# Kernel optimization log

Measured on AMD Instinct MI355X. Metric: run time of the kernel, lower is better.

The kernel has to match this reference:

```python
import jax, jax.numpy as jnp
import numpy as np
from functools import partial

TAU = 2.0          # leak
VTH = 1.0          # threshold_value
DECAY = 1.0 - 1.0 / TAU  # decay_input=False, v_reset=0: v = v*(1-1/tau) + x
PAD = 3
STRIDE = 1


def heaviside(x):
    # forward of spikingjelly surrogate.ATan (surrogate only changes backward)
    return (x >= 0).astype(x.dtype)


def lif(v, inp):
    """One LIF step: charge, fire, hard reset (v_reset=0)."""
    v = v * DECAY + inp
    s = heaviside(v - VTH)
    v = v * (1.0 - s)
    return v, s


def setup_inputs() -> dict:
    key = jax.random.key(0)
    k1, k2, k3, k4 = jax.random.split(key, 4)
    B, L = 64, 2048
    C, H, NC, K = 128, 256, 10, 7
    x = jax.random.normal(k1, (B, L), dtype=jnp.float32)
    conv_w = jax.random.normal(k2, (C, 1, K), dtype=jnp.float32) * (1.0 / np.sqrt(K))
    W1 = jax.random.normal(k3, (H, C), dtype=jnp.float32) * (1.0 / np.sqrt(C))
    W2 = jax.random.normal(k4, (NC, H), dtype=jnp.float32) * (1.0 / np.sqrt(H))
    return {"x": x, "conv_w": conv_w, "W1": W1, "W2": W2}


def _forward(x, conv_w, W1, W2):
    B = x.shape[0]
    C, H, NC = conv_w.shape[0], W1.shape[0], W2.shape[0]
    # Conv1d(1 -> C): [B, 1, L] -> [B, C, T]
    xc = jax.lax.conv_general_dilated(
        x[:, None, :], conv_w, window_strides=(STRIDE,),
        padding=[(PAD, PAD)], dimension_numbers=("NCH", "OIH", "NCH"))
    T = xc.shape[2]
    xt = jnp.transpose(xc, (2, 0, 1))  # [T, B, C]

    def step(carry, x_t):
        v1, v2, v3, acc = carry
        v1, s1 = lif(v1, x_t)                       # conv LIF  [B, C]
        v2, s2 = lif(v2, s1 @ W1.T)                 # hidden LIF [B, H]
        v3, s3 = lif(v3, s2 @ W2.T)                 # output LIF [B, NC]
        return (v1, v2, v3, acc + s3), None

    zeros = lambda d: jnp.zeros((B, d), dtype=x.dtype)
    init = (zeros(C), zeros(H), zeros(NC), zeros(NC))
    (_, _, _, acc), _ = jax.lax.scan(step, init, xt)
    return acc / T


def reference(x, conv_w, W1, W2):
    return _forward(x, conv_w, W1, W2)
```

## Files before the change

### kernel.cpp

```cpp
#include <hip/hip_runtime.h>
#include <stdint.h>

#define T_STEPS 2048
#define BB 64
#define CC 128
#define HH 256
#define NCLS 10

#define S1_OFF  0
#define DP_OFF  16777216
#define DP2_OFF 16908288
#define S2W_OFF 16924672

typedef int v4i __attribute__((ext_vector_type(4)));

__global__ __launch_bounds__(128) void k01_prep(
    const float* __restrict__ x, const float* __restrict__ cw,
    const float* __restrict__ W1, const float* __restrict__ W2,
    unsigned char* __restrict__ s1, signed char* __restrict__ dp,
    signed char* __restrict__ dp2, float* __restrict__ out) {
  const int bx = blockIdx.x;
  const int tidx = threadIdx.x;

  if (bx < 1024) {
    const int c = tidx;
    const int b = bx & 63;
    const int t0 = (bx >> 6) * 128;
    const int ts = t0 - 64;

    float w[7];
#pragma unroll
    for (int k = 0; k < 7; ++k) w[k] = cw[c * 7 + k];

    const float* xb = x + b * 2048;
    float xw[7];
#pragma unroll
    for (int k = 0; k < 7; ++k) {
      int l = ts + k - 3;
      xw[k] = (l >= 0 && l < 2048) ? xb[l] : 0.0f;
    }

    float v = 0.0f;
#pragma unroll 7
    for (int t = ts; t < t0 + 128; ++t) {
      float u = fmaf(w[0], xw[0],
                fmaf(w[1], xw[1],
                fmaf(w[2], xw[2],
                fmaf(w[3], xw[3],
                fmaf(w[4], xw[4],
                fmaf(w[5], xw[5], w[6] * xw[6]))))));
      v = fmaf(v, 0.5f, u);
      bool sp = (v >= 1.0f);
      if (t >= t0) s1[((size_t)t * BB + b) * CC + c] = (unsigned char)(sp ? 1 : 0);
      if (sp) v = 0.0f;
#pragma unroll
      for (int k = 0; k < 6; ++k) xw[k] = xw[k + 1];
      int ln = t + 4;
      xw[6] = (ln >= 0 && ln < 2048) ? xb[ln] : 0.0f;
    }
  } else if (bx < 1280) {
    const int h = bx - 1024;
    const int c = tidx;
    float w = W1[h * CC + c];
    int q = __float2int_rn(w * 2147483648.0f);
#pragma unroll
    for (int d = 0; d < 3; ++d) {
      int dig = (int)(signed char)(q & 0xff);
      dp[d * (HH * CC) + h * CC + c] = (signed char)dig;
      q = (q - dig) >> 8;
    }
    dp[3 * (HH * CC) + h * CC + c] = (signed char)q;
  } else if (bx < 1296) {
    const int nc = bx - 1280;
#pragma unroll
    for (int half = 0; half < 2; ++half) {
      int cc = half * 128 + tidx;
      float w = (nc < NCLS) ? W2[nc * HH + cc] : 0.0f;
      int q = __float2int_rn(w * 2147483648.0f);
#pragma unroll
      for (int d = 0; d < 3; ++d) {
        int dig = (int)(signed char)(q & 0xff);
        dp2[d * (16 * HH) + nc * HH + cc] = (signed char)dig;
        q = (q - dig) >> 8;
      }
      dp2[3 * (16 * HH) + nc * HH + cc] = (signed char)q;
    }
  } else {
#pragma unroll
    for (int i = 0; i < 5; ++i) out[tidx + 128 * i] = 0.0f;
  }
}

__global__ __launch_bounds__(256, 4) void k2_mfma_lif2(
    const unsigned char* __restrict__ s1, const signed char* __restrict__ dp,
    unsigned int* __restrict__ s2w) {
  const int tid  = threadIdx.x;
  const int lane = tid & 63;
  const int wv   = tid >> 6;
  const int hg   = blockIdx.x;
  const int b    = blockIdx.y;
  const int chunk= blockIdx.z;
  const int t0   = chunk * 256;
  const int nwarm= (chunk == 0) ? 0 : 4;
  const int ts   = t0 - nwarm * 16;
  const int l15  = lane & 15;
  const int lg   = lane >> 4;
  const int nn   = lg >> 1;
  const int hb   = hg * 128 + wv * 32;

  v4i Bf[2][4][2];
#pragma unroll
  for (int n = 0; n < 2; ++n)
#pragma unroll
    for (int d = 0; d < 4; ++d)
#pragma unroll
      for (int kc = 0; kc < 2; ++kc)
        Bf[n][d][kc] = *(const v4i*)(dp + d * (HH * CC) +
                                     (hb + n * 16 + l15) * CC + kc * 64 + lg * 16);

  const unsigned char* ap =
      s1 + ((size_t)(ts + l15) * BB + b) * CC + lg * 16;
  v4i Af0 = *(const v4i*)(ap);
  v4i Af1 = *(const v4i*)(ap + 64);
  ap += 16 * BB * CC;

  const int a4 = l15 * 4;
  float v = 0.0f;

  const int nsub = nwarm + 16;
  for (int s = 0; s < nsub; ++s) {
    const int tb = ts + s * 16;

    v4i Pf0 = *(const v4i*)(ap);
    v4i Pf1 = *(const v4i*)(ap + 64);
    ap += 16 * BB * CC;

    float u0[4], u1[4];
#pragma unroll
    for (int n = 0; n < 2; ++n) {
      v4i a0 = {0, 0, 0, 0}, a1 = {0, 0, 0, 0}, a2 = {0, 0, 0, 0}, a3 = {0, 0, 0, 0};
      a0 = __builtin_amdgcn_mfma_i32_16x16x64_i8(Af0, Bf[n][0][0], a0, 0, 0, 0);
      a1 = __builtin_amdgcn_mfma_i32_16x16x64_i8(Af0, Bf[n][1][0], a1, 0, 0, 0);
      a2 = __builtin_amdgcn_mfma_i32_16x16x64_i8(Af0, Bf[n][2][0], a2, 0, 0, 0);
      a3 = __builtin_amdgcn_mfma_i32_16x16x64_i8(Af0, Bf[n][3][0], a3, 0, 0, 0);
      a0 = __builtin_amdgcn_mfma_i32_16x16x64_i8(Af1, Bf[n][0][1], a0, 0, 0, 0);
      a1 = __builtin_amdgcn_mfma_i32_16x16x64_i8(Af1, Bf[n][1][1], a1, 0, 0, 0);
      a2 = __builtin_amdgcn_mfma_i32_16x16x64_i8(Af1, Bf[n][2][1], a2, 0, 0, 0);
      a3 = __builtin_amdgcn_mfma_i32_16x16x64_i8(Af1, Bf[n][3][1], a3, 0, 0, 0);
#pragma unroll
      for (int r = 0; r < 4; ++r) {
        int hi = a3[r] * 256 + a2[r];
        int lo = a1[r] * 256 + a0[r];
        float u = fmaf((float)hi, 0x1p-15f, (float)lo * 0x1p-31f);
        if (n == 0) u0[r] = u; else u1[r] = u;
      }
    }

    float ua[16];
#pragma unroll
    for (int q = 0; q < 4; ++q) {
      const int addr = a4 + q * 64;
#pragma unroll
      for (int r = 0; r < 4; ++r) {
        int g0 = __builtin_amdgcn_ds_bpermute(addr, __float_as_int(u0[r]));
        int g1 = __builtin_amdgcn_ds_bpermute(addr, __float_as_int(u1[r]));
        ua[q * 4 + r] = __int_as_float(nn ? g1 : g0);
      }
    }

    unsigned sel = 0;
#pragma unroll
    for (int j = 0; j < 16; ++j) {
      v = fmaf(v, 0.5f, ua[j]);
      bool sp = (v >= 1.0f);
      if (sp) v = 0.0f;
      unsigned long long Bm = __ballot(sp);
      if (l15 == j)
        sel = (unsigned)(Bm & 0xFFFFull) |
              ((unsigned)((Bm >> 32) & 0xFFFFull) << 16);
    }

    if (s >= nwarm && lg == 0)
      s2w[((size_t)(tb + l15) * BB + b) * 8 + hg * 4 + wv] = sel;

    Af0 = Pf0; Af1 = Pf1;
  }
}

__global__ __launch_bounds__(64, 4) void k34_gemm3_lif3(
    const unsigned int* __restrict__ s2w, const signed char* __restrict__ dp2,
    float* __restrict__ out) {
  const int lane = threadIdx.x;
  const int l15  = lane & 15;
  const int lg   = lane >> 4;
  const int b    = blockIdx.x;
  const int chunk= blockIdx.y;
  const int t0   = chunk * 32;
  const int nwarm= (chunk == 0) ? 0 : 4;
  const int ts   = t0 - nwarm * 16;

  v4i Bf[4][4];
#pragma unroll
  for (int d = 0; d < 4; ++d)
#pragma unroll
    for (int kc = 0; kc < 4; ++kc)
      Bf[d][kc] = *(const v4i*)(dp2 + d * (16 * HH) + l15 * HH + kc * 64 + lg * 16);

  const uint4* rp = (const uint4*)s2w + ((size_t)(ts + l15) * BB + b) * 2;
  uint4 r0 = rp[0], r1 = rp[1];
  rp += 16 * BB * 2;

  const int a4 = l15 * 4;
  const int hw = (lg & 1) * 16;
  float v = 0.0f, cnt = 0.0f;

  const int nsub = nwarm + 2;
  for (int s = 0; s < nsub; ++s) {
    uint4 p0 = rp[0], p1 = rp[1];
    rp += 16 * BB * 2;

    unsigned rowd[8] = {r0.x, r0.y, r0.z, r0.w, r1.x, r1.y, r1.z, r1.w};

    v4i a0 = {0, 0, 0, 0}, a1 = {0, 0, 0, 0}, a2 = {0, 0, 0, 0}, a3 = {0, 0, 0, 0};
#pragma unroll
    for (int kc = 0; kc < 4; ++kc) {
      unsigned h16 = (rowd[kc * 2 + (lg >> 1)] >> hw) & 0xFFFFu;
      v4i Af;
      Af[0] = (int)(((h16 & 0xFu) * 0x00204081u) & 0x01010101u);
      Af[1] = (int)((((h16 >> 4) & 0xFu) * 0x00204081u) & 0x01010101u);
      Af[2] = (int)((((h16 >> 8) & 0xFu) * 0x00204081u) & 0x01010101u);
      Af[3] = (int)((((h16 >> 12) & 0xFu) * 0x00204081u) & 0x01010101u);
      a0 = __builtin_amdgcn_mfma_i32_16x16x64_i8(Af, Bf[0][kc], a0, 0, 0, 0);
      a1 = __builtin_amdgcn_mfma_i32_16x16x64_i8(Af, Bf[1][kc], a1, 0, 0, 0);
      a2 = __builtin_amdgcn_mfma_i32_16x16x64_i8(Af, Bf[2][kc], a2, 0, 0, 0);
      a3 = __builtin_amdgcn_mfma_i32_16x16x64_i8(Af, Bf[3][kc], a3, 0, 0, 0);
    }

    float u[4];
#pragma unroll
    for (int r = 0; r < 4; ++r) {
      int hi = a3[r] * 256 + a2[r];
      int lo = a1[r] * 256 + a0[r];
      u[r] = fmaf((float)hi, 0x1p-15f, (float)lo * 0x1p-31f);
    }

    float ua[16];
#pragma unroll
    for (int q = 0; q < 4; ++q) {
      const int addr = a4 + q * 64;
#pragma unroll
      for (int r = 0; r < 4; ++r)
        ua[q * 4 + r] = __int_as_float(
            __builtin_amdgcn_ds_bpermute(addr, __float_as_int(u[r])));
    }

    float inc = (s >= nwarm) ? 1.0f : 0.0f;
#pragma unroll
    for (int j = 0; j < 16; ++j) {
      v = fmaf(v, 0.5f, ua[j]);
      bool sp = (v >= 1.0f);
      if (sp) { v = 0.0f; cnt += inc; }
    }

    r0 = p0; r1 = p1;
  }

  if (lane < NCLS)
    atomicAdd(&out[b * NCLS + lane], cnt * (1.0f / 2048.0f));
}

extern "C" void kernel_launch(void* const* d_in, const int* in_sizes, int n_in,
                              void* d_out, int out_size, void* d_ws, size_t ws_size,
                              hipStream_t stream) {
  const float* x  = (const float*)d_in[0];
  const float* cw = (const float*)d_in[1];
  const float* W1 = (const float*)d_in[2];
  const float* W2 = (const float*)d_in[3];
  float* out = (float*)d_out;

  char* ws = (char*)d_ws;
  unsigned char* s1  = (unsigned char*)(ws + S1_OFF);
  signed char*   dp  = (signed char*)(ws + DP_OFF);
  signed char*   dp2 = (signed char*)(ws + DP2_OFF);
  unsigned int*  s2w = (unsigned int*)(ws + S2W_OFF);

  k01_prep<<<dim3(1297), 128, 0, stream>>>(x, cw, W1, W2, s1, dp, dp2, out);
  k2_mfma_lif2<<<dim3(2, 64, 8), 256, 0, stream>>>(s1, dp, s2w);
  k34_gemm3_lif3<<<dim3(64, 64), 64, 0, stream>>>(s2w, dp2, out);
  (void)in_sizes; (void)n_in; (void)out_size; (void)ws_size;
}
```

Baseline: 148.4 us.

## Bit-pack layer-1 spikes via ballot and expand them in-register for MFMA

The conv LIF stage now writes spikes as 64-bit ballot masks, one bit per channel, instead of one byte per channel. This shrinks the intermediate spike tensor eightfold. The hidden-layer kernel loads the packed words and expands them to int8 MFMA operands with a multiply-and-mask spread, prefetching two steps ahead. This trades global memory traffic for some extra ALU work in the MFMA kernel, and the workspace offsets are compacted to match.

```diff
diff --git a/kernel.cpp b/kernel.cpp
--- a/kernel.cpp
+++ b/kernel.cpp
@@ -8,22 +8,33 @@
 #define NCLS 10
 
 #define S1_OFF  0
-#define DP_OFF  16777216
-#define DP2_OFF 16908288
-#define S2W_OFF 16924672
+#define DP_OFF  2097152
+#define DP2_OFF 2228224
+#define S2W_OFF 2244608
 
 typedef int v4i __attribute__((ext_vector_type(4)));
+
+__device__ __forceinline__ v4i spread16(unsigned h) {
+  v4i a;
+  a[0] = (int)((((h      ) & 0xFu) * 0x00204081u) & 0x01010101u);
+  a[1] = (int)((((h >> 4 ) & 0xFu) * 0x00204081u) & 0x01010101u);
+  a[2] = (int)((((h >> 8 ) & 0xFu) * 0x00204081u) & 0x01010101u);
+  a[3] = (int)((((h >> 12) & 0xFu) * 0x00204081u) & 0x01010101u);
+  return a;
+}
 
 __global__ __launch_bounds__(128) void k01_prep(
     const float* __restrict__ x, const float* __restrict__ cw,
     const float* __restrict__ W1, const float* __restrict__ W2,
-    unsigned char* __restrict__ s1, signed char* __restrict__ dp,
+    unsigned int* __restrict__ s1b, signed char* __restrict__ dp,
     signed char* __restrict__ dp2, float* __restrict__ out) {
   const int bx = blockIdx.x;
   const int tidx = threadIdx.x;
 
   if (bx < 1024) {
     const int c = tidx;
+    const int wv = tidx >> 6;
+    const int lane = tidx & 63;
     const int b = bx & 63;
     const int t0 = (bx >> 6) * 128;
     const int ts = t0 - 64;
@@ -51,7 +62,9 @@
                 fmaf(w[5], xw[5], w[6] * xw[6]))))));
       v = fmaf(v, 0.5f, u);
       bool sp = (v >= 1.0f);
-      if (t >= t0) s1[((size_t)t * BB + b) * CC + c] = (unsigned char)(sp ? 1 : 0);
+      unsigned long long Bm = __ballot(sp);
+      if (t >= t0 && lane == 0)
+        *(unsigned long long*)(s1b + ((size_t)t * BB + b) * 4 + wv * 2) = Bm;
       if (sp) v = 0.0f;
 #pragma unroll
       for (int k = 0; k < 6; ++k) xw[k] = xw[k + 1];
@@ -92,7 +105,7 @@
 }
 
 __global__ __launch_bounds__(256, 4) void k2_mfma_lif2(
-    const unsigned char* __restrict__ s1, const signed char* __restrict__ dp,
+    const unsigned int* __restrict__ s1b, const signed char* __restrict__ dp,
     unsigned int* __restrict__ s2w) {
   const int tid  = threadIdx.x;
   const int lane = tid & 63;
@@ -107,6 +120,7 @@
   const int lg   = lane >> 4;
   const int nn   = lg >> 1;
   const int hb   = hg * 128 + wv * 32;
+  const int hw   = (lg & 1) * 16;
 
   v4i Bf[2][4][2];
 #pragma unroll
@@ -118,11 +132,10 @@
         Bf[n][d][kc] = *(const v4i*)(dp + d * (HH * CC) +
                                      (hb + n * 16 + l15) * CC + kc * 64 + lg * 16);
 
-  const unsigned char* ap =
-      s1 + ((size_t)(ts + l15) * BB + b) * CC + lg * 16;
-  v4i Af0 = *(const v4i*)(ap);
-  v4i Af1 = *(const v4i*)(ap + 64);
-  ap += 16 * BB * CC;
+  const unsigned int* ap = s1b + ((size_t)(ts + l15) * BB + b) * 4;
+  uint4 Ra = *(const uint4*)ap;
+  uint4 Pb = *(const uint4*)(ap + 16 * BB * 4);
+  const unsigned int* ap2 = ap + 2 * 16 * BB * 4;
 
   const int a4 = l15 * 4;
   float v = 0.0f;
@@ -131,9 +144,13 @@
   for (int s = 0; s < nsub; ++s) {
     const int tb = ts + s * 16;
 
-    v4i Pf0 = *(const v4i*)(ap);
-    v4i Pf1 = *(const v4i*)(ap + 64);
-    ap += 16 * BB * CC;
+    uint4 Pc = *(const uint4*)ap2;
+    ap2 += 16 * BB * 4;
+
+    const unsigned w01 = (lg & 2) ? Ra.y : Ra.x;
+    const unsigned w23 = (lg & 2) ? Ra.w : Ra.z;
+    v4i Af0 = spread16((w01 >> hw) & 0xFFFFu);
+    v4i Af1 = spread16((w23 >> hw) & 0xFFFFu);
 
     float u0[4], u1[4];
 #pragma unroll
@@ -183,7 +200,7 @@
     if (s >= nwarm && lg == 0)
       s2w[((size_t)(tb + l15) * BB + b) * 8 + hg * 4 + wv] = sel;
 
-    Af0 = Pf0; Af1 = Pf1;
+    Ra = Pb; Pb = Pc;
   }
 }
 
@@ -225,11 +242,7 @@
 #pragma unroll
     for (int kc = 0; kc < 4; ++kc) {
       unsigned h16 = (rowd[kc * 2 + (lg >> 1)] >> hw) & 0xFFFFu;
-      v4i Af;
-      Af[0] = (int)(((h16 & 0xFu) * 0x00204081u) & 0x01010101u);
-      Af[1] = (int)((((h16 >> 4) & 0xFu) * 0x00204081u) & 0x01010101u);
-      Af[2] = (int)((((h16 >> 8) & 0xFu) * 0x00204081u) & 0x01010101u);
-      Af[3] = (int)((((h16 >> 12) & 0xFu) * 0x00204081u) & 0x01010101u);
+      v4i Af = spread16(h16);
       a0 = __builtin_amdgcn_mfma_i32_16x16x64_i8(Af, Bf[0][kc], a0, 0, 0, 0);
       a1 = __builtin_amdgcn_mfma_i32_16x16x64_i8(Af, Bf[1][kc], a1, 0, 0, 0);
       a2 = __builtin_amdgcn_mfma_i32_16x16x64_i8(Af, Bf[2][kc], a2, 0, 0, 0);
@@ -279,13 +292,13 @@
   float* out = (float*)d_out;
 
   char* ws = (char*)d_ws;
-  unsigned char* s1  = (unsigned char*)(ws + S1_OFF);
+  unsigned int*  s1b = (unsigned int*)(ws + S1_OFF);
   signed char*   dp  = (signed char*)(ws + DP_OFF);
   signed char*   dp2 = (signed char*)(ws + DP2_OFF);
   unsigned int*  s2w = (unsigned int*)(ws + S2W_OFF);
 
-  k01_prep<<<dim3(1297), 128, 0, stream>>>(x, cw, W1, W2, s1, dp, dp2, out);
-  k2_mfma_lif2<<<dim3(2, 64, 8), 256, 0, stream>>>(s1, dp, s2w);
+  k01_prep<<<dim3(1297), 128, 0, stream>>>(x, cw, W1, W2, s1b, dp, dp2, out);
+  k2_mfma_lif2<<<dim3(2, 64, 8), 256, 0, stream>>>(s1b, dp, s2w);
   k34_gemm3_lif3<<<dim3(64, 64), 64, 0, stream>>>(s2w, dp2, out);
   (void)in_sizes; (void)n_in; (void)out_size; (void)ws_size;
 }
```

Result: slower. 159.8 us (+7.7%).
